# Kernel tuning notes

Measured on AMD Instinct MI355X. Metric: run time of the kernel, lower is better.

## Reference

```python
import jax, jax.numpy as jnp
import numpy as np
import math

D_QKV = 64


def setup_inputs() -> dict:
    key = jax.random.key(0)
    ks = jax.random.split(key, 6)
    b, l, d_model, n_head, d_qkv = 2, 2048, 1024, 16, D_QKV
    return {
        "x": jax.random.normal(ks[0], (b, l, d_model), dtype=jnp.float32),
        "w_q": jax.random.normal(ks[1], (n_head, d_model, d_qkv), dtype=jnp.float32) * (2.0 / (d_model + d_qkv)) ** 0.5,
        "w_k": jax.random.normal(ks[2], (n_head, d_model, d_qkv), dtype=jnp.float32) * (2.0 / (d_model + d_qkv)) ** 0.5,
        "w_v": jax.random.normal(ks[3], (n_head, d_model, d_qkv), dtype=jnp.float32) * (2.0 / (d_model + d_qkv)) ** 0.5,
        "w_o": jax.random.normal(ks[4], (n_head, d_qkv, d_model), dtype=jnp.float32) * (2.0 / (d_model + d_qkv)) ** 0.5,
        "mask": jnp.zeros((b, 1, 1, l), dtype=bool),  # True = masked (padding)
    }


def reference(x, w_q, w_k, w_v, w_o, mask):
    # x: [b, l, m]; w_{q,k,v}: [n, m, d]; w_o: [n, d, m]; mask broadcastable to [b, n, l, l]
    q = jnp.einsum("blm,nmd->bnld", x, w_q)
    k = jnp.einsum("blm,nmd->bnld", x, w_k)
    v = jnp.einsum("blm,nmd->bnld", x, w_v)
    scores = jnp.einsum("bnld,bnkd->bnlk", q, k) / math.sqrt(D_QKV)
    scores = jnp.where(mask, jnp.float32(-1e9), scores)
    attn = jax.nn.softmax(scores, axis=-1)  # dropout is identity (p=0 / eval)
    ctx = jnp.einsum("bnlk,bnkd->bnld", attn, v)
    # per-head output projection then sum over heads: V.matmul(w_o).sum(dim=1)
    return jnp.einsum("bnld,ndm->blm", ctx, w_o)
```

## Files before the change

kernel.cpp:

```cpp
#include <hip/hip_runtime.h>
#include <stdint.h>

using bf16x8  = __attribute__((ext_vector_type(8))) short;
using f32x4   = __attribute__((ext_vector_type(4))) float;
using f32x16  = __attribute__((ext_vector_type(16))) float;
using ushort8 = __attribute__((ext_vector_type(8))) unsigned short;
using ushort4v= __attribute__((ext_vector_type(4))) unsigned short;
using uint2v  = __attribute__((ext_vector_type(2))) unsigned int;

typedef __attribute__((address_space(1))) const unsigned int* gas_ptr;
typedef __attribute__((address_space(3))) unsigned int*       las_ptr;

__device__ __forceinline__ void gload_lds16(const unsigned short* g, unsigned short* l) {
    __builtin_amdgcn_global_load_lds((gas_ptr)(const void*)g, (las_ptr)(void*)l, 16, 0, 0);
}

__device__ __forceinline__ unsigned short f2bf(float f) {
    union { float f; uint32_t u; } x; x.f = f;
    uint32_t u = x.u;
    uint32_t r = u + 0x7fffu + ((u >> 16) & 1u);
    return (unsigned short)(r >> 16);
}
__device__ __forceinline__ float bf2f(unsigned short u) {
    union { uint32_t u; float f; } x; x.u = ((uint32_t)u) << 16;
    return x.f;
}

__device__ __forceinline__ f32x4 mfma16(bf16x8 a, bf16x8 b, f32x4 c) {
    return __builtin_amdgcn_mfma_f32_16x16x32_bf16(a, b, c, 0, 0, 0);
}
__device__ __forceinline__ f32x16 mfma32(bf16x8 a, bf16x8 b, f32x16 c) {
    return __builtin_amdgcn_mfma_f32_32x32x16_bf16(a, b, c, 0, 0, 0);
}

__device__ __forceinline__ unsigned int cvtpk_bf16(float lo, float hi) {
    unsigned int r;
    asm("v_cvt_pk_bf16_f32 %0, %1, %2" : "=v"(r) : "v"(lo), "v"(hi));
    return r;
}
__device__ __forceinline__ void plswap(unsigned int& a, unsigned int& b) {
    asm("v_permlane32_swap_b32 %0, %1" : "+v"(a), "+v"(b));
}


__global__ void cast_x_kernel(const float* __restrict__ x, unsigned short* __restrict__ xb) {
    int i = blockIdx.x * 256 + threadIdx.x;
    using f32x4v = __attribute__((ext_vector_type(4))) float;
    f32x4v v = ((const f32x4v*)x)[i];
    ushort4v o;
    o[0] = f2bf(v[0]); o[1] = f2bf(v[1]); o[2] = f2bf(v[2]); o[3] = f2bf(v[3]);
    ((ushort4v*)xb)[i] = o;
}

__global__ void pack_wqkv_t(const float* __restrict__ wq, const float* __restrict__ wk,
                            const float* __restrict__ wv, unsigned short* __restrict__ wpT) {
    __shared__ float tile[64][65];
    const int mm = blockIdx.y;
    const int s = mm >> 4, hh = mm & 15;
    const float* src = ((s == 0) ? wq : (s == 1) ? wk : wv) + (size_t)hh * 1024 * 64;
    const int k0 = blockIdx.x * 64;
    const int c = threadIdx.x & 63, rg = threadIdx.x >> 6;
#pragma unroll
    for (int i = 0; i < 16; ++i) {
        int r = rg * 16 + i;
        tile[r][c] = src[(size_t)(k0 + r) * 64 + c];
    }
    __syncthreads();
    unsigned short* dst = wpT + ((size_t)s * 1024 + hh * 64) * 1024 + k0;
    const int kc = threadIdx.x & 63, dg = threadIdx.x >> 6;
#pragma unroll
    for (int i = 0; i < 16; ++i) {
        int d = dg * 16 + i;
        dst[(size_t)d * 1024 + kc] = f2bf(tile[kc][d]);
    }
}

__global__ void pack_wo_t(const float* __restrict__ wo, unsigned short* __restrict__ woT) {
    __shared__ float tile[64][65];
    const int r0 = blockIdx.y * 64;
    const int c0 = blockIdx.x * 64;
    const int c = threadIdx.x & 63, rg = threadIdx.x >> 6;
#pragma unroll
    for (int i = 0; i < 16; ++i) {
        int r = rg * 16 + i;
        tile[r][c] = wo[(size_t)(r0 + r) * 1024 + c0 + c];
    }
    __syncthreads();
    const int kc = threadIdx.x & 63, mg = threadIdx.x >> 6;
#pragma unroll
    for (int i = 0; i < 16; ++i) {
        int m = mg * 16 + i;
        woT[(size_t)(c0 + m) * 1024 + r0 + kc] = f2bf(tile[kc][m]);
    }
}


template<int MODE, int BN>
__global__ __launch_bounds__(256) void gemm_bt(
    const unsigned short* __restrict__ A,
    const unsigned short* __restrict__ BT,
    float* __restrict__ Cf,
    unsigned short* __restrict__ Q,
    unsigned short* __restrict__ Kq,
    unsigned short* __restrict__ V,
    int M, int N, int K)
{
    constexpr int NF = BN / 32;
    __shared__ unsigned short As[128 * 64];
    __shared__ unsigned short Bs[BN * 64];
    const int tid  = threadIdx.x;
    const int lane = tid & 63;
    const int wave = tid >> 6;
    const int wm = wave >> 1, wn = wave & 1;
    const int l15 = lane & 15, l4 = lane >> 4;
    const int row0 = blockIdx.y * 128;
    const int col0 = blockIdx.x * BN;

    f32x4 acc[4][NF];
#pragma unroll
    for (int i = 0; i < 4; ++i)
#pragma unroll
        for (int j = 0; j < NF; ++j) acc[i][j] = (f32x4){0.f, 0.f, 0.f, 0.f};

    for (int k0 = 0; k0 < K; k0 += 64) {
        __syncthreads();
#pragma unroll
        for (int it = 0; it < 4; ++it) {
            int cb = (it * 4 + wave) * 64;
            int c  = cb + lane;
            int r  = c >> 3, c8 = c & 7;
            int sc8 = c8 ^ (r & 7);
            gload_lds16(&A[(size_t)(row0 + r) * K + k0 + sc8 * 8], &As[cb * 8]);
        }
#pragma unroll
        for (int it = 0; it < NF; ++it) {
            int cb = (it * 4 + wave) * 64;
            int c  = cb + lane;
            int r  = c >> 3, c8 = c & 7;
            int sc8 = c8 ^ (r & 7);
            gload_lds16(&BT[(size_t)(col0 + r) * K + k0 + sc8 * 8], &Bs[cb * 8]);
        }
        __syncthreads();
#pragma unroll
        for (int kk = 0; kk < 2; ++kk) {
            bf16x8 af[4], bfr[NF];
#pragma unroll
            for (int m = 0; m < 4; ++m) {
                int r   = wm * 64 + m * 16 + l15;
                int blk = (kk * 4 + l4) ^ (r & 7);
                af[m] = *(const bf16x8*)&As[r * 64 + blk * 8];
            }
#pragma unroll
            for (int n = 0; n < NF; ++n) {
                int r   = wn * (BN / 2) + n * 16 + l15;
                int blk = (kk * 4 + l4) ^ (r & 7);
                bfr[n] = *(const bf16x8*)&Bs[r * 64 + blk * 8];
            }
#pragma unroll
            for (int m = 0; m < 4; ++m)
#pragma unroll
                for (int n = 0; n < NF; ++n)
                    acc[m][n] = mfma16(af[m], bfr[n], acc[m][n]);
        }
    }

#pragma unroll
    for (int m = 0; m < 4; ++m) {
#pragma unroll
        for (int n = 0; n < NF; ++n) {
#pragma unroll
            for (int r = 0; r < 4; ++r) {
                int gr = row0 + wm * 64 + m * 16 + l4 * 4 + r;
                int gc = col0 + wn * (BN / 2) + n * 16 + l15;
                float v = acc[m][n][r];
                if (MODE == 0) {
                    int s = gc >> 10, rem = gc & 1023;
                    int hh = rem >> 6, dd = rem & 63;
                    int bb = gr >> 11, ll = gr & 2047;
                    unsigned short* dst = (s == 0) ? Q : (s == 1) ? Kq : V;
                    dst[(((size_t)bb * 16 + hh) * 2048 + ll) * 64 + dd] = f2bf(v);
                } else {
                    Cf[(size_t)gr * N + gc] = v;
                }
            }
        }
    }
}


__global__ __launch_bounds__(256) void attn_kernel(
    const unsigned short* __restrict__ qb,
    const unsigned short* __restrict__ kb,
    const unsigned short* __restrict__ vb,
    const unsigned char* __restrict__ mask,
    unsigned short* __restrict__ part0,
    unsigned short* __restrict__ part1,
    float* __restrict__ ml)
{
    const int lg = blockIdx.x;
    int u = ((lg & 7) << 7) | (lg >> 3);
    int bh = u >> 5, sub = u & 31;
    const int qt = sub >> 1, half = sub & 1;
    const int b = bh >> 4, h = bh & 15;
    const int t0 = half * 16;
    const int NT = 16;

    const int tid  = threadIdx.x;
    const int lane = tid & 63, wave = tid >> 6;
    const int l31  = lane & 31, hi = lane >> 5;

    __shared__ unsigned short smem[16384];
    __shared__ int flags[32];

    const size_t hoff = ((size_t)(b * 16 + h)) * 2048 * 64;
    const unsigned short* qh = qb + hoff;
    const unsigned short* kh = kb + hoff;
    const unsigned short* vh = vb + hoff;
    const unsigned char*  mb = mask + (size_t)b * 2048;

    if (tid < 32) flags[tid] = 0;
    __syncthreads();
    {
        uint2v mv = *(const uint2v*)&mb[tid * 8];
        if (mv[0] | mv[1]) flags[tid >> 3] = 1;
    }

    const int qrow = qt * 128 + wave * 32 + l31;
    bf16x8 qf[4];
#pragma unroll
    for (int ki = 0; ki < 4; ++ki)
        qf[ki] = *(const bf16x8*)&qh[(size_t)qrow * 64 + ki * 16 + hi * 8];

    f32x16 accA = {0,0,0,0,0,0,0,0,0,0,0,0,0,0,0,0};
    f32x16 accB = {0,0,0,0,0,0,0,0,0,0,0,0,0,0,0,0};
    float m_r = -1e30f, l_r = 0.f;
    const float SC  = 0.18033688011112042f;
    const float THR = 44.3614195558365f;

    const int krow = tid >> 3, kc16 = tid & 7;
    const int vd = tid & 63, vcb = (tid >> 6) * 2;

    ushort8 kreg[2];
    unsigned short vreg[16];
    {
        const int kvb = t0 * 64;
#pragma unroll
        for (int it = 0; it < 2; ++it)
            kreg[it] = *(const ushort8*)&kh[(size_t)(kvb + krow + it * 32) * 64 + kc16 * 8];
#pragma unroll
        for (int j = 0; j < 16; ++j)
            vreg[j] = vh[(size_t)(kvb + vcb * 8 + j) * 64 + vd];
    }

    for (int t = t0; t < t0 + NT; ++t) {
        const int kv0 = t * 64;
        unsigned short* Kb = smem + (t & 1) * 4096;
        unsigned short* Vb = smem + 8192 + (t & 1) * 4096;

#pragma unroll
        for (int it = 0; it < 2; ++it) {
            int r = krow + it * 32;
            *(ushort8*)&Kb[r * 64 + ((kc16 ^ (r & 7)) * 8)] = kreg[it];
        }
        {
            union { unsigned short u[16]; ushort8 v[2]; } p;
#pragma unroll
            for (int j = 0; j < 16; ++j) p.u[j] = vreg[j];
#pragma unroll
            for (int c = 0; c < 2; ++c) {
                int cc = vcb + c;
                *(ushort8*)&Vb[vd * 64 + ((cc ^ (vd & 7)) * 8)] = p.v[c];
            }
        }
        __syncthreads();

        if (t < t0 + NT - 1) {
            const int kvn = kv0 + 64;
#pragma unroll
            for (int it = 0; it < 2; ++it)
                kreg[it] = *(const ushort8*)&kh[(size_t)(kvn + krow + it * 32) * 64 + kc16 * 8];
#pragma unroll
            for (int j = 0; j < 16; ++j)
                vreg[j] = vh[(size_t)(kvn + vcb * 8 + j) * 64 + vd];
        }

        f32x16 s0 = {0,0,0,0,0,0,0,0,0,0,0,0,0,0,0,0};
        f32x16 s1 = {0,0,0,0,0,0,0,0,0,0,0,0,0,0,0,0};
        __builtin_amdgcn_s_setprio(1);
#pragma unroll
        for (int ki = 0; ki < 4; ++ki) {
            int c0 = ((ki * 2 + hi) ^ (l31 & 7)) * 8;
            bf16x8 a0 = *(const bf16x8*)&Kb[l31 * 64 + c0];
            bf16x8 a1 = *(const bf16x8*)&Kb[(32 + l31) * 64 + c0];
            s0 = mfma32(a0, qf[ki], s0);
            s1 = mfma32(a1, qf[ki], s1);
        }
        __builtin_amdgcn_s_setprio(0);

        if (flags[t]) {
#pragma unroll
            for (int r = 0; r < 16; ++r) {
                int keyl = (r & 3) + 8 * (r >> 2) + 4 * hi;
                if (mb[kv0 + keyl])      s0[r] = -1e30f;
                if (mb[kv0 + 32 + keyl]) s1[r] = -1e30f;
            }
        }

        float mx;
        {
            float a0 = fmaxf(fmaxf(s0[0], s0[1]),  fmaxf(s0[2],  s0[3]));
            float a1 = fmaxf(fmaxf(s0[4], s0[5]),  fmaxf(s0[6],  s0[7]));
            float a2 = fmaxf(fmaxf(s0[8], s0[9]),  fmaxf(s0[10], s0[11]));
            float a3 = fmaxf(fmaxf(s0[12], s0[13]), fmaxf(s0[14], s0[15]));
            float b0 = fmaxf(fmaxf(s1[0], s1[1]),  fmaxf(s1[2],  s1[3]));
            float b1 = fmaxf(fmaxf(s1[4], s1[5]),  fmaxf(s1[6],  s1[7]));
            float b2 = fmaxf(fmaxf(s1[8], s1[9]),  fmaxf(s1[10], s1[11]));
            float b3 = fmaxf(fmaxf(s1[12], s1[13]), fmaxf(s1[14], s1[15]));
            mx = fmaxf(fmaxf(fmaxf(a0, a1), fmaxf(a2, a3)),
                       fmaxf(fmaxf(b0, b1), fmaxf(b2, b3)));
        }
        mx = fmaxf(mx, __shfl_xor(mx, 32));
        if (__any(mx > m_r + THR)) {
            float mn  = fmaxf(m_r, mx);
            float scl = __builtin_amdgcn_exp2f((m_r - mn) * SC);
            m_r = mn;
            l_r *= scl;
#pragma unroll
            for (int i = 0; i < 16; ++i) { accA[i] *= scl; accB[i] *= scl; }
        }
        const float nmc = -m_r * SC;
#pragma unroll
        for (int i = 0; i < 16; ++i) {
            s0[i] = __builtin_amdgcn_exp2f(__builtin_fmaf(s0[i], SC, nmc));
            s1[i] = __builtin_amdgcn_exp2f(__builtin_fmaf(s1[i], SC, nmc));
        }
        float rs;
        {
            float a0 = (s0[0] + s0[1]) + (s0[2] + s0[3]);
            float a1 = (s0[4] + s0[5]) + (s0[6] + s0[7]);
            float a2 = (s0[8] + s0[9]) + (s0[10] + s0[11]);
            float a3 = (s0[12] + s0[13]) + (s0[14] + s0[15]);
            float b0 = (s1[0] + s1[1]) + (s1[2] + s1[3]);
            float b1 = (s1[4] + s1[5]) + (s1[6] + s1[7]);
            float b2 = (s1[8] + s1[9]) + (s1[10] + s1[11]);
            float b3 = (s1[12] + s1[13]) + (s1[14] + s1[15]);
            rs = ((a0 + a1) + (a2 + a3)) + ((b0 + b1) + (b2 + b3));
        }
        rs += __shfl_xor(rs, 32);
        l_r += rs;

        bf16x8 pf[4];
        {
            union { unsigned int u[4]; bf16x8 v; } f;
            unsigned int w0 = cvtpk_bf16(s0[0],  s0[1]),  w1 = cvtpk_bf16(s0[2],  s0[3]);
            unsigned int w2 = cvtpk_bf16(s0[4],  s0[5]),  w3 = cvtpk_bf16(s0[6],  s0[7]);
            unsigned int w4 = cvtpk_bf16(s0[8],  s0[9]),  w5 = cvtpk_bf16(s0[10], s0[11]);
            unsigned int w6 = cvtpk_bf16(s0[12], s0[13]), w7 = cvtpk_bf16(s0[14], s0[15]);
            plswap(w0, w2); plswap(w1, w3); plswap(w4, w6); plswap(w5, w7);
            f.u[0] = w0; f.u[1] = w1; f.u[2] = w2; f.u[3] = w3; pf[0] = f.v;
            f.u[0] = w4; f.u[1] = w5; f.u[2] = w6; f.u[3] = w7; pf[1] = f.v;
            unsigned int x0 = cvtpk_bf16(s1[0],  s1[1]),  x1 = cvtpk_bf16(s1[2],  s1[3]);
            unsigned int x2 = cvtpk_bf16(s1[4],  s1[5]),  x3 = cvtpk_bf16(s1[6],  s1[7]);
            unsigned int x4 = cvtpk_bf16(s1[8],  s1[9]),  x5 = cvtpk_bf16(s1[10], s1[11]);
            unsigned int x6 = cvtpk_bf16(s1[12], s1[13]), x7 = cvtpk_bf16(s1[14], s1[15]);
            plswap(x0, x2); plswap(x1, x3); plswap(x4, x6); plswap(x5, x7);
            f.u[0] = x0; f.u[1] = x1; f.u[2] = x2; f.u[3] = x3; pf[2] = f.v;
            f.u[0] = x4; f.u[1] = x5; f.u[2] = x6; f.u[3] = x7; pf[3] = f.v;
        }

        __builtin_amdgcn_s_setprio(1);
#pragma unroll
        for (int ks = 0; ks < 4; ++ks) {
            int c0 = ((ks * 2 + hi) ^ (l31 & 7)) * 8;
            bf16x8 vA = *(const bf16x8*)&Vb[l31 * 64 + c0];
            bf16x8 vB = *(const bf16x8*)&Vb[(32 + l31) * 64 + c0];
            accA = mfma32(vA, pf[ks], accA);
            accB = mfma32(vB, pf[ks], accB);
        }
        __builtin_amdgcn_s_setprio(0);
    }

    __syncthreads();
    const int qloc = wave * 32 + l31;
#pragma unroll
    for (int r = 0; r < 16; ++r) {
        int dA = (r & 3) + 8 * (r >> 2) + 4 * hi;
        smem[qloc * 64 + (dA ^ ((qloc & 7) * 8))]        = f2bf(accA[r]);
        smem[qloc * 64 + ((32 + dA) ^ ((qloc & 7) * 8))] = f2bf(accB[r]);
    }
    if (hi == 0) {
        size_t mrow = ((size_t)half * 32 + b * 16 + h) * 2048 + qt * 128 + qloc;
        *(float2*)&ml[mrow * 2] = make_float2(m_r, l_r);
    }
    __syncthreads();
    unsigned short* pdst = half ? part1 : part0;
    const size_t prow0 = ((size_t)(b * 16 + h)) * 2048 + qt * 128;
#pragma unroll
    for (int it = 0; it < 4; ++it) {
        int idx = tid + it * 256;
        int q = idx >> 3, c = idx & 7;
        ushort8 vv = *(const ushort8*)&smem[q * 64 + ((c * 8) ^ ((q & 7) * 8))];
        *(ushort8*)&pdst[(prow0 + q) * 64 + c * 8] = vv;
    }
}


__global__ void combine_kernel(const unsigned short* __restrict__ part0,
                               const unsigned short* __restrict__ part1,
                               const float* __restrict__ ml,
                               unsigned short* __restrict__ ctxb)
{
    const float SC = 0.18033688011112042f;
    int gid = blockIdx.x * 256 + threadIdx.x;
    int row = gid >> 3, c = gid & 7;
    ushort8 v0 = *(const ushort8*)&part0[(size_t)row * 64 + c * 8];
    ushort8 v1 = *(const ushort8*)&part1[(size_t)row * 64 + c * 8];
    float2 a = *(const float2*)&ml[(size_t)row * 2];
    float2 d = *(const float2*)&ml[(size_t)(65536 + row) * 2];
    float m  = fmaxf(a.x, d.x);
    float w0 = __builtin_amdgcn_exp2f((a.x - m) * SC);
    float w1 = __builtin_amdgcn_exp2f((d.x - m) * SC);
    float li = 1.0f / (a.y * w0 + d.y * w1);
    ushort8 o;
#pragma unroll
    for (int j = 0; j < 8; ++j)
        o[j] = f2bf((bf2f(v0[j]) * w0 + bf2f(v1[j]) * w1) * li);
    int bh = row >> 11, ql = row & 2047;
    int bb = bh >> 4, hh = bh & 15;
    *(ushort8*)&ctxb[((size_t)(bb * 2048 + ql)) * 1024 + hh * 64 + c * 8] = o;
}


extern "C" void kernel_launch(void* const* d_in, const int* in_sizes, int n_in,
                              void* d_out, int out_size, void* d_ws, size_t ws_size,
                              hipStream_t stream)
{
    const float* x  = (const float*)d_in[0];
    const float* wq = (const float*)d_in[1];
    const float* wk = (const float*)d_in[2];
    const float* wv = (const float*)d_in[3];
    const float* wo = (const float*)d_in[4];
    const unsigned char* mask = (const unsigned char*)d_in[5];
    float* out = (float*)d_out;

    char* ws = (char*)d_ws;
    unsigned short* xb   = (unsigned short*)(ws);
    unsigned short* wpT  = (unsigned short*)(ws + 8388608);
    unsigned short* woT  = (unsigned short*)(ws + 14680064);
    unsigned short* qb   = (unsigned short*)(ws + 16777216);
    unsigned short* kb   = (unsigned short*)(ws + 25165824);
    unsigned short* vb   = (unsigned short*)(ws + 33554432);
    unsigned short* ctxb = (unsigned short*)(ws + 41943040);
    unsigned short* part0 = xb;
    unsigned short* part1 = (unsigned short*)d_out;
    float*          mlb   = (float*)((char*)d_out + 8388608);

    cast_x_kernel<<<4096, 256, 0, stream>>>(x, xb);
    pack_wqkv_t  <<<dim3(16, 48), 256, 0, stream>>>(wq, wk, wv, wpT);
    pack_wo_t    <<<dim3(16, 16), 256, 0, stream>>>(wo, woT);

    gemm_bt<0,128><<<dim3(24, 32), 256, 0, stream>>>(xb, wpT, nullptr, qb, kb, vb, 4096, 3072, 1024);

    attn_kernel<<<1024, 256, 0, stream>>>(qb, kb, vb, mask, part0, part1, mlb);
    combine_kernel<<<2048, 256, 0, stream>>>(part0, part1, mlb, ctxb);

    gemm_bt<1,64><<<dim3(16, 32), 256, 0, stream>>>(ctxb, woT, out, nullptr, nullptr, nullptr, 4096, 1024, 1024);
}
```

Before: 135.6 us.

## Pre-transpose V and stage K/V tiles with direct global-to-LDS loads

Adds a separate kernel that transposes V per head into a d-major layout. The attention kernel then loads both K and V tiles straight into LDS with swizzled global_load_lds calls instead of going through registers. This removes the strided 2-byte V gathers and the register staging, and the kernel now requests an occupancy hint of 4 blocks per multiprocessor. The cost is an extra launch plus one more round trip of V through memory, and workspace buffers are reassigned so the partial outputs and softmax stats live in the output and weight-pack regions.

```diff
diff --git a/kernel.cpp b/kernel.cpp
--- a/kernel.cpp
+++ b/kernel.cpp
@@ -91,6 +91,30 @@
     for (int i = 0; i < 16; ++i) {
         int m = mg * 16 + i;
         woT[(size_t)(c0 + m) * 1024 + r0 + kc] = f2bf(tile[kc][m]);
+    }
+}
+
+__global__ void vt_kernel(const unsigned short* __restrict__ vb, unsigned short* __restrict__ vtb) {
+    __shared__ unsigned short tile[64][72];
+    const int bh = blockIdx.y;
+    const int l0 = blockIdx.x * 64;
+    const unsigned short* src = vb + (size_t)bh * 131072;
+    unsigned short* dst = vtb + (size_t)bh * 131072;
+    const int c8 = threadIdx.x & 7, r2 = threadIdx.x >> 3;
+#pragma unroll
+    for (int it = 0; it < 2; ++it) {
+        int r = r2 + it * 32;
+        ushort8 v = *(const ushort8*)&src[(size_t)(l0 + r) * 64 + c8 * 8];
+        *(ushort8*)&tile[r][c8 * 8] = v;
+    }
+    __syncthreads();
+#pragma unroll
+    for (int it = 0; it < 2; ++it) {
+        int d = r2 + it * 32;
+        ushort8 o;
+#pragma unroll
+        for (int j = 0; j < 8; ++j) o[j] = tile[c8 * 8 + j][d];
+        *(ushort8*)&dst[(size_t)d * 2048 + l0 + c8 * 8] = o;
     }
 }
 
@@ -188,10 +212,10 @@
 }
 
 
-__global__ __launch_bounds__(256) void attn_kernel(
+__global__ __launch_bounds__(256, 4) void attn_kernel(
     const unsigned short* __restrict__ qb,
     const unsigned short* __restrict__ kb,
-    const unsigned short* __restrict__ vb,
+    const unsigned short* __restrict__ vtb,
     const unsigned char* __restrict__ mask,
     unsigned short* __restrict__ part0,
     unsigned short* __restrict__ part1,
@@ -212,11 +236,11 @@
     __shared__ unsigned short smem[16384];
     __shared__ int flags[32];
 
-    const size_t hoff = ((size_t)(b * 16 + h)) * 2048 * 64;
-    const unsigned short* qh = qb + hoff;
-    const unsigned short* kh = kb + hoff;
-    const unsigned short* vh = vb + hoff;
-    const unsigned char*  mb = mask + (size_t)b * 2048;
+    const size_t hoff = (size_t)bh * 131072;
+    const unsigned short* qh  = qb  + hoff;
+    const unsigned short* kh  = kb  + hoff;
+    const unsigned short* vth = vtb + hoff;
+    const unsigned char*  mb  = mask + (size_t)b * 2048;
 
     if (tid < 32) flags[tid] = 0;
     __syncthreads();
@@ -237,51 +261,30 @@
     const float SC  = 0.18033688011112042f;
     const float THR = 44.3614195558365f;
 
-    const int krow = tid >> 3, kc16 = tid & 7;
-    const int vd = tid & 63, vcb = (tid >> 6) * 2;
-
-    ushort8 kreg[2];
-    unsigned short vreg[16];
-    {
-        const int kvb = t0 * 64;
-#pragma unroll
-        for (int it = 0; it < 2; ++it)
-            kreg[it] = *(const ushort8*)&kh[(size_t)(kvb + krow + it * 32) * 64 + kc16 * 8];
-#pragma unroll
-        for (int j = 0; j < 16; ++j)
-            vreg[j] = vh[(size_t)(kvb + vcb * 8 + j) * 64 + vd];
-    }
+#define STAGE(KB, VB, KV0) do {                                                          \
+        _Pragma("unroll")                                                                \
+        for (int it_ = 0; it_ < 2; ++it_) {                                              \
+            int c_ = it_ * 256 + tid;                                                    \
+            int r_ = c_ >> 3, c8_ = c_ & 7;                                              \
+            int sc8_ = c8_ ^ (r_ & 7);                                                   \
+            gload_lds16(&kh[(size_t)((KV0) + r_) * 64 + sc8_ * 8],                       \
+                        &(KB)[(it_ * 256 + wave * 64) * 8]);                             \
+            gload_lds16(&vth[(size_t)r_ * 2048 + (KV0) + sc8_ * 8],                      \
+                        &(VB)[(it_ * 256 + wave * 64) * 8]);                             \
+        }                                                                                \
+    } while (0)
+
+    STAGE(smem, smem + 8192, t0 * 64);
 
     for (int t = t0; t < t0 + NT; ++t) {
         const int kv0 = t * 64;
-        unsigned short* Kb = smem + (t & 1) * 4096;
-        unsigned short* Vb = smem + 8192 + (t & 1) * 4096;
-
-#pragma unroll
-        for (int it = 0; it < 2; ++it) {
-            int r = krow + it * 32;
-            *(ushort8*)&Kb[r * 64 + ((kc16 ^ (r & 7)) * 8)] = kreg[it];
-        }
-        {
-            union { unsigned short u[16]; ushort8 v[2]; } p;
-#pragma unroll
-            for (int j = 0; j < 16; ++j) p.u[j] = vreg[j];
-#pragma unroll
-            for (int c = 0; c < 2; ++c) {
-                int cc = vcb + c;
-                *(ushort8*)&Vb[vd * 64 + ((cc ^ (vd & 7)) * 8)] = p.v[c];
-            }
-        }
+        unsigned short* Kb = smem + ((t - t0) & 1) * 4096;
+        unsigned short* Vb = smem + 8192 + ((t - t0) & 1) * 4096;
         __syncthreads();
-
-        if (t < t0 + NT - 1) {
-            const int kvn = kv0 + 64;
-#pragma unroll
-            for (int it = 0; it < 2; ++it)
-                kreg[it] = *(const ushort8*)&kh[(size_t)(kvn + krow + it * 32) * 64 + kc16 * 8];
-#pragma unroll
-            for (int j = 0; j < 16; ++j)
-                vreg[j] = vh[(size_t)(kvn + vcb * 8 + j) * 64 + vd];
+        if (t + 1 < t0 + NT) {
+            unsigned short* Kn = smem + ((t + 1 - t0) & 1) * 4096;
+            unsigned short* Vn = smem + 8192 + ((t + 1 - t0) & 1) * 4096;
+            STAGE(Kn, Vn, kv0 + 64);
         }
 
         f32x16 s0 = {0,0,0,0,0,0,0,0,0,0,0,0,0,0,0,0};
@@ -379,6 +382,7 @@
         }
         __builtin_amdgcn_s_setprio(0);
     }
+#undef STAGE
 
     __syncthreads();
     const int qloc = wave * 32 + l31;
@@ -389,12 +393,12 @@
         smem[qloc * 64 + ((32 + dA) ^ ((qloc & 7) * 8))] = f2bf(accB[r]);
     }
     if (hi == 0) {
-        size_t mrow = ((size_t)half * 32 + b * 16 + h) * 2048 + qt * 128 + qloc;
+        size_t mrow = ((size_t)half * 32 + bh) * 2048 + qt * 128 + qloc;
         *(float2*)&ml[mrow * 2] = make_float2(m_r, l_r);
     }
     __syncthreads();
     unsigned short* pdst = half ? part1 : part0;
-    const size_t prow0 = ((size_t)(b * 16 + h)) * 2048 + qt * 128;
+    const size_t prow0 = (size_t)bh * 2048 + qt * 128;
 #pragma unroll
     for (int it = 0; it < 4; ++it) {
         int idx = tid + it * 256;
@@ -451,9 +455,10 @@
     unsigned short* kb   = (unsigned short*)(ws + 25165824);
     unsigned short* vb   = (unsigned short*)(ws + 33554432);
     unsigned short* ctxb = (unsigned short*)(ws + 41943040);
-    unsigned short* part0 = xb;
-    unsigned short* part1 = (unsigned short*)d_out;
-    float*          mlb   = (float*)((char*)d_out + 8388608);
+    unsigned short* vtb   = xb;
+    unsigned short* part0 = (unsigned short*)d_out;
+    unsigned short* part1 = (unsigned short*)d_out + 4194304;
+    float*          mlb   = (float*)wpT;
 
     cast_x_kernel<<<4096, 256, 0, stream>>>(x, xb);
     pack_wqkv_t  <<<dim3(16, 48), 256, 0, stream>>>(wq, wk, wv, wpT);
@@ -461,7 +466,8 @@
 
     gemm_bt<0,128><<<dim3(24, 32), 256, 0, stream>>>(xb, wpT, nullptr, qb, kb, vb, 4096, 3072, 1024);
 
-    attn_kernel<<<1024, 256, 0, stream>>>(qb, kb, vb, mask, part0, part1, mlb);
+    vt_kernel<<<dim3(32, 32), 256, 0, stream>>>(vb, vtb);
+    attn_kernel<<<1024, 256, 0, stream>>>(qb, kb, vtb, mask, part0, part1, mlb);
     combine_kernel<<<2048, 256, 0, stream>>>(part0, part1, mlb, ctxb);
 
     gemm_bt<1,64><<<dim3(16, 32), 256, 0, stream>>>(ctxb, woT, out, nullptr, nullptr, nullptr, 4096, 1024, 1024);
```

Result: no change. 133.4 us (-1.6%).
